# Kernel optimization log

Hardware: AMD Instinct MI355X
Metric: run time of the kernel (lower is better)

## Reference

```python
import jax, jax.numpy as jnp
import numpy as np

POS_MARGIN = 0.9   # sample_method on
NEG_MARGIN = 0.1
EPOCH_NUM = 300
BASE = 0.5


def setup_inputs() -> dict:
    key = jax.random.key(0)
    k1, k2 = jax.random.split(key)
    n, d = 8192, 128
    x = jax.random.normal(k1, (n, d), dtype=jnp.float32)
    x = x / jnp.linalg.norm(x, axis=1, keepdims=True)  # L2-normalized embeddings
    targets = jax.random.randint(k2, (n,), 0, 100, dtype=jnp.int64 if jax.config.jax_enable_x64 else jnp.int32)
    return {"inputs": x, "targets": targets, "nonorm": 0}


def reference(inputs, targets, nonorm):
    n = inputs.shape[0]
    ep = EPOCH_NUM / 300.0  # dynamic-margin coefficient
    sim = inputs @ inputs.T  # [n, n]
    eq = targets[:, None] == targets[None, :]

    # positive pairs: same label and sim < pos_margin
    pos_mask = eq & (sim < POS_MARGIN)
    pos_min = jnp.min(jnp.where(pos_mask, sim, jnp.inf), axis=1)  # min(pos_pair_) per row

    # negative pairs: diff label, sim + 0.5 > min(pos), sim > neg_margin
    neg_mask = (~eq) & (sim + BASE > pos_min[:, None]) & (sim > NEG_MARGIN)

    pos_term = jnp.where(pos_mask, jnp.exp(-2.0 * (sim - BASE) + ep * (sim - POS_MARGIN) ** 2), 0.0)
    pos_loss = 0.5 * jnp.log1p(pos_term.sum(axis=1))
    neg_term = jnp.where(neg_mask, jnp.exp(50.0 * (sim - BASE) + ep * (NEG_MARGIN - sim) ** 2), 0.0)
    neg_loss = (1.0 / 50.0) * jnp.log1p(neg_term.sum(axis=1))

    has_neg = neg_mask.any(axis=1)  # rows with empty neg set are skipped
    loss = jnp.where(has_neg, pos_loss + neg_loss, 0.0).sum() / n
    prec = jnp.mean((~has_neg).astype(jnp.float32))

    # mean_pos_sim / mean_neg_sim come from the LAST row's filtered pairs
    last_pos = pos_mask[n - 1]
    last_neg = neg_mask[n - 1]
    mean_pos_sim = jnp.sum(jnp.where(last_pos, sim[n - 1], 0.0)) / jnp.maximum(last_pos.sum(), 1)
    mean_neg_sim = jnp.sum(jnp.where(last_neg, sim[n - 1], 0.0)) / jnp.maximum(last_neg.sum(), 1)
    return (loss, prec, mean_pos_sim, mean_neg_sim)
```

## Files before the change

### kernel.cpp

```cpp
#include <hip/hip_runtime.h>
#include <hip/hip_bf16.h>
#include <math.h>


#define D 128
#define NL 128
#define POSB NL

typedef __attribute__((ext_vector_type(8))) short short8;
typedef __attribute__((ext_vector_type(4))) float float4v;

__device__ inline float waveSum(float v) {
    #pragma unroll
    for (int o = 32; o > 0; o >>= 1) v += __shfl_down(v, o, 64);
    return v;
}
__device__ inline float waveMin(float v) {
    #pragma unroll
    for (int o = 32; o > 0; o >>= 1) v = fminf(v, __shfl_down(v, o, 64));
    return v;
}

__device__ inline void load_lds16(const void* g, void* l) {
    __builtin_amdgcn_global_load_lds(
        (const __attribute__((address_space(1))) unsigned int*)g,
        (__attribute__((address_space(3))) unsigned int*)l, 16, 0, 0);
}

__global__ __launch_bounds__(1024) void prep_kernel(
    const float* __restrict__ x, ushort* __restrict__ xb, int total8,
    const int* __restrict__ t, int* __restrict__ offs, int* __restrict__ list,
    float* __restrict__ part, float* __restrict__ last4,
    float* __restrict__ out, int n, int nconv)
{
    const int tid = threadIdx.x;
    const int bx = blockIdx.x;
    if (bx < nconv) {
        const int g = bx * 1024 + tid;
        if (g >= total8) return;
        const float4* src = (const float4*)(x) + g * 2;
        float4 a = src[0], b = src[1];
        float f[8] = {a.x, a.y, a.z, a.w, b.x, b.y, b.z, b.w};
        ushort r[8];
        #pragma unroll
        for (int i = 0; i < 8; ++i) {
            unsigned u = __float_as_uint(f[i]);
            r[i] = (ushort)((u + 0x7FFFu + ((u >> 16) & 1u)) >> 16);
        }
        uint4 packed;
        packed.x = (unsigned)r[0] | ((unsigned)r[1] << 16);
        packed.y = (unsigned)r[2] | ((unsigned)r[3] << 16);
        packed.z = (unsigned)r[4] | ((unsigned)r[5] << 16);
        packed.w = (unsigned)r[6] | ((unsigned)r[7] << 16);
        ((uint4*)xb)[g] = packed;
        return;
    }
    if (bx > nconv) {
        const int zb = bx - nconv - 1;
        const int g4 = zb * 4096 + tid * 4;
        if (g4 < 8 * n)
            *(float4*)(part + g4) = (float4){0.f, 0.f, 0.f, 0.f};
        return;
    }
    __shared__ int cnt[NL], cur[NL];
    if (tid < 4) { last4[tid] = 0.f; out[tid] = 0.f; }
    if (tid < NL) cnt[tid] = 0;
    __syncthreads();
    for (int j = tid; j < n; j += 1024) atomicAdd(&cnt[t[j]], 1);
    __syncthreads();
    if (tid == 0) {
        int acc = 0;
        for (int g = 0; g < NL; ++g) { cur[g] = acc; offs[g] = acc; acc += cnt[g]; }
        offs[NL] = acc;
    }
    __syncthreads();
    for (int j = tid; j < n; j += 1024) {
        int p = atomicAdd(&cur[t[j]], 1);
        list[p] = j;
    }
}

__global__ __launch_bounds__(256, 3) void fused_kernel(
    const ushort* __restrict__ xb,
    const int* __restrict__ t,
    const int* __restrict__ offs, const int* __restrict__ list,
    float* __restrict__ pos_min, float* __restrict__ pos_sum,
    float* __restrict__ part, float* __restrict__ last4, int n, int ntri)
{
    __shared__ __align__(16) unsigned char smem[32768 + 2048];
    const int tid = threadIdx.x;
    const int bx = blockIdx.x;

    const int w = tid >> 6, lane = tid & 63;
    const int wy = w >> 1, wx = w & 1;
    const int quad = lane >> 4, lq = lane & 15;

    if (bx >= POSB) {
        int b = bx - POSB;
        int r = (int)((sqrtf(8.0f * (float)b + 1.0f) - 1.0f) * 0.5f);
        while ((r + 1) * (r + 2) / 2 <= b) ++r;
        while (r * (r + 1) / 2 > b) --r;
        const int c = b - r * (r + 1) / 2;
        const bool offdiag = (r != c);

        const int i0 = r * 128, j0 = c * 128;
        const bool has_last = (i0 == n - 128);

        int* labr = (int*)(smem + 32768);
        int* labc = labr + 128;
        for (int l = tid; l < 128; l += 256) {
            labr[l] = t[i0 + l];
            labc[l] = t[j0 + l];
        }

        uint4* Au = (uint4*)smem;
        uint4* Bu = Au + 128 * 8;
        const uint4* xbv = (const uint4*)xb;
        const short8* As = (const short8*)Au;
        const short8* Bs = (const short8*)Bu;

        float4v acc[4][4];
        #pragma unroll
        for (int a = 0; a < 4; ++a)
            #pragma unroll
            for (int d2 = 0; d2 < 4; ++d2) acc[a][d2] = (float4v){0.f, 0.f, 0.f, 0.f};

        #pragma unroll
        for (int h = 0; h < 2; ++h) {
            if (h) __syncthreads();
            #pragma unroll
            for (int it = 0; it < 4; ++it) {
                const int d = tid + it * 256;
                const int row = d >> 3;
                const int q = (d & 7) ^ (row & 7);
                const int ub = (d & ~63) * 16;
                load_lds16(xbv + (size_t)(i0 + row) * 16 + h * 8 + q,
                           (char*)Au + ub);
                load_lds16(xbv + (size_t)(j0 + row) * 16 + h * 8 + q,
                           (char*)Bu + ub);
            }
            __syncthreads();
            #pragma unroll
            for (int s = 0; s < 2; ++s) {
                short8 af[4], bf[4];
                #pragma unroll
                for (int tt = 0; tt < 4; ++tt) {
                    const int ra = wy * 64 + tt * 16 + lq;
                    const int rb2 = wx * 64 + tt * 16 + lq;
                    af[tt] = As[ra * 8 + ((s * 4 + quad) ^ (lq & 7))];
                    bf[tt] = Bs[rb2 * 8 + ((s * 4 + quad) ^ (lq & 7))];
                }
                #pragma unroll
                for (int tr = 0; tr < 4; ++tr)
                    #pragma unroll
                    for (int tc = 0; tc < 4; ++tc)
                        acc[tr][tc] = __builtin_amdgcn_mfma_f32_16x16x32_bf16(
                            af[tr], bf[tc], acc[tr][tc], 0, 0, 0);
            }
        }
        __syncthreads();

        float* pp_r = (float*)smem;
        float* pp_c = ((float*)smem) + 32 * 129;

        int lcv[4];
        #pragma unroll
        for (int tc = 0; tc < 4; ++tc) lcv[tc] = labc[wx * 64 + tc * 16 + lq];
        float colp[4] = {0.f, 0.f, 0.f, 0.f};

        #pragma unroll
        for (int tr = 0; tr < 4; ++tr) {
            #pragma unroll
            for (int reg = 0; reg < 4; ++reg) {
                const int row_loc = wy * 64 + tr * 16 + quad * 4 + reg;
                const int lr = labr[row_loc];
                float ns = 0.f;
                #pragma unroll
                for (int tc = 0; tc < 4; ++tc) {
                    const float s = acc[tr][tc][reg];
                    const bool sel = (lr != lcv[tc]) & (s > 0.1f);
                    const float e = sel
                        ? __expf(fmaf(s, s, fmaf(49.8f, s, -24.99f))) : 0.f;
                    ns += e; colp[tc] += e;
                }
                pp_r[(wx * 16 + lq) * 129 + row_loc] = ns;

                if (has_last && (i0 + row_loc == n - 1)) {
                    float ssim = 0.f, ncf = 0.f;
                    #pragma unroll
                    for (int tc = 0; tc < 4; ++tc) {
                        const float s = acc[tr][tc][reg];
                        if ((lr != lcv[tc]) & (s > 0.1f)) { ssim += s; ncf += 1.f; }
                    }
                    #pragma unroll
                    for (int o = 1; o < 16; o <<= 1) {
                        ssim += __shfl_xor(ssim, o, 64);
                        ncf  += __shfl_xor(ncf, o, 64);
                    }
                    if (lq == 0 && ncf > 0.f) {
                        atomicAdd(&last4[2], ssim);
                        atomicAdd(&last4[3], ncf);
                    }
                }
            }
        }
        if (offdiag) {
            #pragma unroll
            for (int tc = 0; tc < 4; ++tc)
                pp_c[(wy * 4 + quad) * 129 + (wx * 64 + tc * 16 + lq)] = colp[tc];
        }
        __syncthreads();

        if (tid < 128) {
            float s = 0.f;
            #pragma unroll
            for (int cc = 0; cc < 32; ++cc) s += pp_r[cc * 129 + tid];
            atomicAdd(&part[(size_t)(c & 7) * n + i0 + tid], s);
            if (offdiag) {
                float s2 = 0.f;
                #pragma unroll
                for (int cc = 0; cc < 8; ++cc) s2 += pp_c[cc * 129 + tid];
                atomicAdd(&part[(size_t)(r & 7) * n + j0 + tid], s2);
            }
        }
        return;
    }

    const int g = bx;
    const int s0 = offs[g], m = offs[g + 1] - s0;
    if (m <= 0) return;

    uint4* Au = (uint4*)smem;
    uint4* Bu = Au + 128 * 8;
    const uint4* xbv = (const uint4*)xb;
    const short8* As = (const short8*)Au;
    const short8* Bs = (const short8*)Bu;
    int* lrow = (int*)(smem + 33280);
    int* lcol = lrow + 128;

    const int lastlab = t[n - 1];
    const bool glast = (g == lastlab);
    const int nrt = (m + 127) >> 7;

    for (int rt = 0; rt < nrt; ++rt) {
        const int rbase = rt << 7;
        const int rleft = min(128, m - rbase);
        for (int ct = 0; ct < nrt; ++ct) {
            const int cbase = ct << 7;
            __syncthreads();
            for (int l = tid; l < 128; l += 256) {
                lrow[l] = list[s0 + min(rbase + l, m - 1)];
                lcol[l] = list[s0 + min(cbase + l, m - 1)];
            }
            __syncthreads();

            float4v acc[4][4];
            #pragma unroll
            for (int a = 0; a < 4; ++a)
                #pragma unroll
                for (int d2 = 0; d2 < 4; ++d2) acc[a][d2] = (float4v){0.f, 0.f, 0.f, 0.f};

            #pragma unroll
            for (int h = 0; h < 2; ++h) {
                if (h) __syncthreads();
                #pragma unroll
                for (int it = 0; it < 4; ++it) {
                    const int d = tid + it * 256;
                    const int row = d >> 3;
                    const int q = (d & 7) ^ (row & 7);
                    const int ub = (d & ~63) * 16;
                    load_lds16(xbv + (size_t)lrow[row] * 16 + h * 8 + q,
                               (char*)Au + ub);
                    load_lds16(xbv + (size_t)lcol[row] * 16 + h * 8 + q,
                               (char*)Bu + ub);
                }
                __syncthreads();
                #pragma unroll
                for (int ks = 0; ks < 2; ++ks) {
                    short8 af[4], bf[4];
                    #pragma unroll
                    for (int tt = 0; tt < 4; ++tt) {
                        const int ra = wy * 64 + tt * 16 + lq;
                        const int rb2 = wx * 64 + tt * 16 + lq;
                        af[tt] = As[ra * 8 + ((ks * 4 + quad) ^ (lq & 7))];
                        bf[tt] = Bs[rb2 * 8 + ((ks * 4 + quad) ^ (lq & 7))];
                    }
                    #pragma unroll
                    for (int tr = 0; tr < 4; ++tr)
                        #pragma unroll
                        for (int tc = 0; tc < 4; ++tc)
                            acc[tr][tc] = __builtin_amdgcn_mfma_f32_16x16x32_bf16(
                                af[tr], bf[tc], acc[tr][tc], 0, 0, 0);
                }
            }
            __syncthreads();

            float* pp_s = (float*)smem;
            float* pp_m = ((float*)smem) + 32 * 129;
            float ssl = 0.f, scl = 0.f;
            bool hadlast = false;

            #pragma unroll
            for (int tr = 0; tr < 4; ++tr) {
                #pragma unroll
                for (int reg = 0; reg < 4; ++reg) {
                    const int row_loc = wy * 64 + tr * 16 + quad * 4 + reg;
                    float ps = 0.f, mn = INFINITY;
                    #pragma unroll
                    for (int tc = 0; tc < 4; ++tc) {
                        const int col = cbase + wx * 64 + tc * 16 + lq;
                        const float sv = acc[tr][tc][reg];
                        const bool val = (col < m) & (sv < 0.9f);
                        mn = fminf(mn, val ? sv : INFINITY);
                        ps += val ? __expf(fmaf(sv, sv, fmaf(-3.8f, sv, 1.81f))) : 0.f;
                    }
                    pp_s[(wx * 16 + lq) * 129 + row_loc] = ps;
                    pp_m[(wx * 16 + lq) * 129 + row_loc] = mn;

                    if (glast && row_loc < rleft && lrow[row_loc] == n - 1) {
                        hadlast = true;
                        #pragma unroll
                        for (int tc = 0; tc < 4; ++tc) {
                            const int col = cbase + wx * 64 + tc * 16 + lq;
                            const float sv = acc[tr][tc][reg];
                            if ((col < m) & (sv < 0.9f)) { ssl += sv; scl += 1.f; }
                        }
                    }
                }
            }
            if (glast) {
                #pragma unroll
                for (int o = 1; o < 16; o <<= 1) {
                    ssl += __shfl_xor(ssl, o, 64);
                    scl += __shfl_xor(scl, o, 64);
                }
                if (hadlast && lq == 0) {
                    atomicAdd(&last4[0], ssl);
                    atomicAdd(&last4[1], scl);
                }
            }
            __syncthreads();

            if (tid < rleft) {
                float sres = 0.f, mres = INFINITY;
                #pragma unroll
                for (int cc = 0; cc < 32; ++cc) {
                    sres += pp_s[cc * 129 + tid];
                    mres = fminf(mres, pp_m[cc * 129 + tid]);
                }
                const int i = lrow[tid];
                if (ct == 0) { pos_sum[i] = sres; pos_min[i] = mres; }
                else {
                    pos_sum[i] += sres;
                    pos_min[i] = fminf(pos_min[i], mres);
                }
            }
        }
    }
}

__global__ __launch_bounds__(256) void finalize_kernel(
    const ushort* __restrict__ xb, const int* __restrict__ t,
    const float* __restrict__ pos_min, const float* __restrict__ pos_sum,
    const float* __restrict__ part, const float* __restrict__ last4,
    float* __restrict__ out, int n)
{
    const int tid = threadIdx.x;
    const int base = blockIdx.x * 256;
    const int i = base + tid;
    const float pm = pos_min[i];
    const bool flag = (pm > 0.6f);

    __shared__ int fl[256];
    __shared__ int nfl, lastflag;
    __shared__ float corr[256];
    __shared__ float xi2[D];
    __shared__ float red[3][4];
    __shared__ float lastst[2];
    if (tid == 0) { nfl = 0; lastflag = 0; }
    __syncthreads();
    if (flag) { int q = atomicAdd(&nfl, 1); fl[q] = tid; }
    __syncthreads();
    const int m = nfl;

    for (int e = 0; e < m; ++e) {
        const int lr_ = fl[e];
        const int ri = base + lr_;
        if (tid < D)
            xi2[tid] = __uint_as_float(((unsigned)xb[(size_t)ri * D + tid]) << 16);
        __syncthreads();
        const float pth = fmaxf(0.1f, pos_min[ri] - 0.5f);
        const int lab = t[ri];
        float S = 0.f, ss = 0.f, cnt = 0.f;
        for (int j = tid; j < n; j += 256) {
            if (t[j] == lab) continue;
            float d = 0.f;
            const ushort* xr = xb + (size_t)j * D;
            for (int q = 0; q < D; ++q)
                d += __uint_as_float(((unsigned)xr[q]) << 16) * xi2[q];
            if (d > pth) {
                S += __expf(fmaf(d, d, fmaf(49.8f, d, -24.99f)));
                ss += d; cnt += 1.f;
            }
        }
        const int lane = tid & 63, wv = tid >> 6;
        S = waveSum(S); ss = waveSum(ss); cnt = waveSum(cnt);
        if (lane == 0) { red[0][wv] = S; red[1][wv] = ss; red[2][wv] = cnt; }
        __syncthreads();
        if (tid == 0) {
            corr[lr_] = red[0][0] + red[0][1] + red[0][2] + red[0][3];
            if (ri == n - 1) {
                lastst[0] = red[1][0] + red[1][1] + red[1][2] + red[1][3];
                lastst[1] = red[2][0] + red[2][1] + red[2][2] + red[2][3];
                lastflag = 1;
            }
        }
        __syncthreads();
    }

    float s;
    if (flag) {
        s = corr[tid];
    } else {
        s = 0.f;
        #pragma unroll
        for (int sl = 0; sl < 8; ++sl) s += part[(size_t)sl * n + i];
    }
    float l = 0.f, nno = 0.f;
    if (s > 0.f)
        l = 0.5f * log1pf(pos_sum[i]) + 0.02f * log1pf(s);
    else
        nno = 1.f;
    const int lane = tid & 63, wv = tid >> 6;
    l = waveSum(l); nno = waveSum(nno);
    __syncthreads();
    if (lane == 0) { red[0][wv] = l; red[1][wv] = nno; }
    __syncthreads();
    if (tid == 0) {
        float L = red[0][0] + red[0][1] + red[0][2] + red[0][3];
        float P = red[1][0] + red[1][1] + red[1][2] + red[1][3];
        atomicAdd(&out[0], L / (float)n);
        atomicAdd(&out[1], P / (float)n);
    }
    if (i == n - 1) {
        out[2] = last4[0] / fmaxf(last4[1], 1.f);
        float a = lastflag ? lastst[0] : last4[2];
        float b2 = lastflag ? lastst[1] : last4[3];
        out[3] = a / fmaxf(b2, 1.f);
    }
}

extern "C" void kernel_launch(void* const* d_in, const int* in_sizes, int n_in,
                              void* d_out, int out_size, void* d_ws, size_t ws_size,
                              hipStream_t stream) {
    const float* x = (const float*)d_in[0];
    const int*   t = (const int*)d_in[1];
    const int n = in_sizes[1];

    float* ws      = (float*)d_ws;
    float* pos_min = ws;
    float* pos_sum = ws + n;
    float* last4   = ws + 2 * n;
    float* part    = ws + 2 * n + 4;
    int*   offs    = (int*)(ws + 10 * n + 4);
    int*   list    = (int*)(ws + 10 * n + 4 + NL + 1);
    size_t xb_off  = ((size_t)(11 * n + 4 + NL + 1) + 3) & ~(size_t)3;
    ushort* xb     = (ushort*)(ws + xb_off);

    const int total8 = n * D / 8;
    const int nconv = (total8 + 1023) / 1024;
    const int nzero = (8 * n + 4095) / 4096;
    prep_kernel<<<nconv + 1 + nzero, 1024, 0, stream>>>(
        x, xb, total8, t, offs, list, part, last4, (float*)d_out, n, nconv);

    const int nb = n / 128;
    const int ntri = nb * (nb + 1) / 2;
    fused_kernel<<<POSB + ntri, 256, 0, stream>>>(
        xb, t, offs, list, pos_min, pos_sum, part, last4, n, ntri);

    finalize_kernel<<<n / 256, 256, 0, stream>>>(xb, t, pos_min, pos_sum,
                                                 part, last4, (float*)d_out, n);
}
```

Measured before the change: 94.40 us.

## Prefetch second K-half into registers and replace LDS row/col reduction with shuffles

In the triangle-tile path, the first half of K is loaded into LDS asynchronously. The second half is loaded into registers at the same time, so its global latency overlaps the first half's MFMA work; it is then written to LDS after a barrier. The LDS partial-sum staging and its final barrier are replaced by wave shuffle reductions with direct atomicAdds into the partial buffer. This roughly doubles the number of global atomics and adds eight uint4 registers of pressure under a 3-blocks-per-CU launch bound.

```diff
diff --git a/kernel.cpp b/kernel.cpp
--- a/kernel.cpp
+++ b/kernel.cpp
@@ -13,11 +13,6 @@
 __device__ inline float waveSum(float v) {
     #pragma unroll
     for (int o = 32; o > 0; o >>= 1) v += __shfl_down(v, o, 64);
-    return v;
-}
-__device__ inline float waveMin(float v) {
-    #pragma unroll
-    for (int o = 32; o > 0; o >>= 1) v = fminf(v, __shfl_down(v, o, 64));
     return v;
 }
 
@@ -85,7 +80,7 @@
     const int* __restrict__ t,
     const int* __restrict__ offs, const int* __restrict__ list,
     float* __restrict__ pos_min, float* __restrict__ pos_sum,
-    float* __restrict__ part, float* __restrict__ last4, int n, int ntri)
+    float* __restrict__ part, float* __restrict__ last4, int n)
 {
     __shared__ __align__(16) unsigned char smem[32768 + 2048];
     const int tid = threadIdx.x;
@@ -119,49 +114,74 @@
         const short8* As = (const short8*)Au;
         const short8* Bs = (const short8*)Bu;
 
+        #pragma unroll
+        for (int it = 0; it < 4; ++it) {
+            const int d = tid + it * 256;
+            const int row = d >> 3;
+            const int q = (d & 7) ^ (row & 7);
+            const int ub = (d & ~63) * 16;
+            load_lds16(xbv + (size_t)(i0 + row) * 16 + q, (char*)Au + ub);
+            load_lds16(xbv + (size_t)(j0 + row) * 16 + q, (char*)Bu + ub);
+        }
+        uint4 pre[8];
+        #pragma unroll
+        for (int it = 0; it < 4; ++it) {
+            const int d = tid + it * 256;
+            const int row = d >> 3;
+            const int q = (d & 7) ^ (row & 7);
+            pre[it * 2]     = xbv[(size_t)(i0 + row) * 16 + 8 + q];
+            pre[it * 2 + 1] = xbv[(size_t)(j0 + row) * 16 + 8 + q];
+        }
+
         float4v acc[4][4];
         #pragma unroll
         for (int a = 0; a < 4; ++a)
             #pragma unroll
             for (int d2 = 0; d2 < 4; ++d2) acc[a][d2] = (float4v){0.f, 0.f, 0.f, 0.f};
 
-        #pragma unroll
-        for (int h = 0; h < 2; ++h) {
-            if (h) __syncthreads();
-            #pragma unroll
-            for (int it = 0; it < 4; ++it) {
-                const int d = tid + it * 256;
-                const int row = d >> 3;
-                const int q = (d & 7) ^ (row & 7);
-                const int ub = (d & ~63) * 16;
-                load_lds16(xbv + (size_t)(i0 + row) * 16 + h * 8 + q,
-                           (char*)Au + ub);
-                load_lds16(xbv + (size_t)(j0 + row) * 16 + h * 8 + q,
-                           (char*)Bu + ub);
-            }
-            __syncthreads();
-            #pragma unroll
-            for (int s = 0; s < 2; ++s) {
-                short8 af[4], bf[4];
-                #pragma unroll
-                for (int tt = 0; tt < 4; ++tt) {
-                    const int ra = wy * 64 + tt * 16 + lq;
-                    const int rb2 = wx * 64 + tt * 16 + lq;
-                    af[tt] = As[ra * 8 + ((s * 4 + quad) ^ (lq & 7))];
-                    bf[tt] = Bs[rb2 * 8 + ((s * 4 + quad) ^ (lq & 7))];
-                }
-                #pragma unroll
-                for (int tr = 0; tr < 4; ++tr)
-                    #pragma unroll
-                    for (int tc = 0; tc < 4; ++tc)
-                        acc[tr][tc] = __builtin_amdgcn_mfma_f32_16x16x32_bf16(
-                            af[tr], bf[tc], acc[tr][tc], 0, 0, 0);
-            }
-        }
-        __syncthreads();
-
-        float* pp_r = (float*)smem;
-        float* pp_c = ((float*)smem) + 32 * 129;
+        __syncthreads();
+        #pragma unroll
+        for (int s = 0; s < 2; ++s) {
+            short8 af[4], bf[4];
+            #pragma unroll
+            for (int tt = 0; tt < 4; ++tt) {
+                const int ra = wy * 64 + tt * 16 + lq;
+                const int rb2 = wx * 64 + tt * 16 + lq;
+                af[tt] = As[ra * 8 + ((s * 4 + quad) ^ (lq & 7))];
+                bf[tt] = Bs[rb2 * 8 + ((s * 4 + quad) ^ (lq & 7))];
+            }
+            #pragma unroll
+            for (int tr = 0; tr < 4; ++tr)
+                #pragma unroll
+                for (int tc = 0; tc < 4; ++tc)
+                    acc[tr][tc] = __builtin_amdgcn_mfma_f32_16x16x32_bf16(
+                        af[tr], bf[tc], acc[tr][tc], 0, 0, 0);
+        }
+        __syncthreads();
+        #pragma unroll
+        for (int it = 0; it < 4; ++it) {
+            const int d = tid + it * 256;
+            *(uint4*)((char*)Au + d * 16) = pre[it * 2];
+            *(uint4*)((char*)Bu + d * 16) = pre[it * 2 + 1];
+        }
+        __syncthreads();
+        #pragma unroll
+        for (int s = 0; s < 2; ++s) {
+            short8 af[4], bf[4];
+            #pragma unroll
+            for (int tt = 0; tt < 4; ++tt) {
+                const int ra = wy * 64 + tt * 16 + lq;
+                const int rb2 = wx * 64 + tt * 16 + lq;
+                af[tt] = As[ra * 8 + ((s * 4 + quad) ^ (lq & 7))];
+                bf[tt] = Bs[rb2 * 8 + ((s * 4 + quad) ^ (lq & 7))];
+            }
+            #pragma unroll
+            for (int tr = 0; tr < 4; ++tr)
+                #pragma unroll
+                for (int tc = 0; tc < 4; ++tc)
+                    acc[tr][tc] = __builtin_amdgcn_mfma_f32_16x16x32_bf16(
+                        af[tr], bf[tc], acc[tr][tc], 0, 0, 0);
+        }
 
         int lcv[4];
         #pragma unroll
@@ -183,7 +203,6 @@
                         ? __expf(fmaf(s, s, fmaf(49.8f, s, -24.99f))) : 0.f;
                     ns += e; colp[tc] += e;
                 }
-                pp_r[(wx * 16 + lq) * 129 + row_loc] = ns;
 
                 if (has_last && (i0 + row_loc == n - 1)) {
                     float ssim = 0.f, ncf = 0.f;
@@ -202,25 +221,21 @@
                         atomicAdd(&last4[3], ncf);
                     }
                 }
+
+                #pragma unroll
+                for (int o = 1; o < 16; o <<= 1) ns += __shfl_xor(ns, o, 64);
+                if (lq == 0)
+                    atomicAdd(&part[(size_t)(c & 7) * n + i0 + row_loc], ns);
             }
         }
         if (offdiag) {
             #pragma unroll
-            for (int tc = 0; tc < 4; ++tc)
-                pp_c[(wy * 4 + quad) * 129 + (wx * 64 + tc * 16 + lq)] = colp[tc];
-        }
-        __syncthreads();
-
-        if (tid < 128) {
-            float s = 0.f;
-            #pragma unroll
-            for (int cc = 0; cc < 32; ++cc) s += pp_r[cc * 129 + tid];
-            atomicAdd(&part[(size_t)(c & 7) * n + i0 + tid], s);
-            if (offdiag) {
-                float s2 = 0.f;
-                #pragma unroll
-                for (int cc = 0; cc < 8; ++cc) s2 += pp_c[cc * 129 + tid];
-                atomicAdd(&part[(size_t)(r & 7) * n + j0 + tid], s2);
+            for (int tc = 0; tc < 4; ++tc) {
+                float v = colp[tc];
+                v += __shfl_xor(v, 16, 64);
+                v += __shfl_xor(v, 32, 64);
+                if (lane < 16)
+                    atomicAdd(&part[(size_t)(r & 7) * n + j0 + wx * 64 + tc * 16 + lane], v);
             }
         }
         return;
@@ -476,7 +491,7 @@
     const int nb = n / 128;
     const int ntri = nb * (nb + 1) / 2;
     fused_kernel<<<POSB + ntri, 256, 0, stream>>>(
-        xb, t, offs, list, pos_min, pos_sum, part, last4, n, ntri);
+        xb, t, offs, list, pos_min, pos_sum, part, last4, n);
 
     finalize_kernel<<<n / 256, 256, 0, stream>>>(xb, t, pos_min, pos_sum,
                                                  part, last4, (float*)d_out, n);
```

After: 153.5 us. +62.6%, slower.
